# Kernel tuning notes

Hardware: AMD Instinct MI355X
Metric: run time of the kernel (lower is better)

The kernel has to match this reference:

```python
import jax, jax.numpy as jnp
import numpy as np

NUM_TOKENS = 8192
MODEL_DIM = 4096
NUM_EXPERTS = 64
CAPACITY_FACTOR = 1.0


def setup_inputs() -> dict:
    key = jax.random.key(0)
    k1, k2 = jax.random.split(key)
    inp = jax.random.normal(k1, (NUM_TOKENS, MODEL_DIM), dtype=jnp.float32)
    wg = jax.random.normal(k2, (NUM_EXPERTS, MODEL_DIM), dtype=jnp.float32) * (1.0 / np.sqrt(MODEL_DIM))
    return {"input": inp, "wg_weight": wg}


def reference(input, wg_weight):
    # logits = input @ wg.T  -> [T, E]
    logits = jnp.einsum('td,ed->te', input, wg_weight)
    num_tokens, num_experts = logits.shape
    capacity = int(CAPACITY_FACTOR * ((num_tokens + num_experts - 1) // num_experts))

    indices1_s = jnp.argmax(logits, axis=1)                      # [T]
    mask1 = jax.nn.one_hot(indices1_s, num_experts, dtype=logits.dtype)  # [T, E]
    gates = jax.nn.softmax(logits, axis=1)                       # [T, E]
    gates1_s = jnp.sum(gates * mask1, axis=1)                    # [T]

    # locations: position of each token within its chosen expert's queue
    # (exclusive cumsum over the one-hot mask, gathered at the chosen expert)
    locations1 = jnp.cumsum(mask1, axis=0) - 1.0                 # [T, E]
    locations1_s = jnp.sum(locations1 * mask1, axis=1).astype(jnp.int32)  # [T]

    # load-balancing aux loss (float32 branch of the original)
    me = jnp.sum(gates, axis=0)                                  # [E]
    ce = jnp.sum(mask1, axis=0)                                  # [E]
    l_aux = jnp.sum(me * ce) * (num_experts / (num_tokens * num_tokens))

    return (l_aux, indices1_s.astype(jnp.int32), locations1_s, gates1_s)
```

## Files before the change

kernel.cpp:

```cpp
#include <hip/hip_runtime.h>

namespace {
constexpr int TOK = 8192;
constexpr int DIM = 4096;
constexpr int NE  = 64;
constexpr int TB  = 128;
constexpr int KS  = 8;
constexpr int KR  = DIM / KS;
constexpr int NKS = KR / 32;
constexpr int TOTKS = DIM / 32;
constexpr int NT  = TOK / TB;
constexpr int GB  = 64;
constexpr int NCH = TOK / GB;
}

typedef _Float16 f16x8 __attribute__((ext_vector_type(8)));
typedef float    f32x4 __attribute__((ext_vector_type(4)));

__global__ __launch_bounds__(256) void prepack_w(
    const float* __restrict__ W, f16x8* __restrict__ whi,
    f16x8* __restrict__ wlo) {
  const int gid = blockIdx.x * 256 + threadIdx.x;
  const int lane = gid & 63;
  const int gk   = (gid >> 6) & (TOTKS - 1);
  const int et   = gid >> 13;
  const int e = et * 16 + (lane & 15);
  const int k = gk * 32 + (lane >> 4) * 8;
  const float4 r0 = *(const float4*)(W + (size_t)e * DIM + k);
  const float4 r1 = *(const float4*)(W + (size_t)e * DIM + k + 4);
  f16x8 hi, lo;
  const float rv[8] = {r0.x, r0.y, r0.z, r0.w, r1.x, r1.y, r1.z, r1.w};
#pragma unroll
  for (int j = 0; j < 8; ++j) {
    const _Float16 h = (_Float16)rv[j];
    hi[j] = h;
    lo[j] = (_Float16)(rv[j] - (float)h);
  }
  whi[gid] = hi;
  wlo[gid] = lo;
}

__global__ __launch_bounds__(512, 4) void gemm_split(
    const float* __restrict__ A, const _Float16* __restrict__ whi,
    const _Float16* __restrict__ wlo, float* __restrict__ partial) {
  __shared__ _Float16 sB[8 * 8 * 64 * 8];

  const int bid  = blockIdx.x;
  const int tile = bid & (NT - 1);
  const int ks   = bid / NT;
  const int t0   = tile * TB;
  const int tid  = threadIdx.x;
  const int w    = tid >> 6;
  const int lane = tid & 63;
  const int col  = lane & 15;
  const int quad = lane >> 4;
  const int gk0  = ks * NKS;

  const float* Ap = A + (size_t)(t0 + w * 16 + col) * DIM + ks * KR + quad * 8;

  f32x4 acc[4];
#pragma unroll
  for (int et = 0; et < 4; ++et) acc[et] = (f32x4)0.0f;

  float4 a0  = *(const float4*)(Ap);
  float4 a1  = *(const float4*)(Ap + 4);
  float4 a0n = *(const float4*)(Ap + 32);
  float4 a1n = *(const float4*)(Ap + 36);

  const _Float16* src_base =
      ((w < 4) ? whi : wlo) + ((size_t)((w & 3) * TOTKS + gk0) << 9);
  _Float16* dst_base = sB + ((size_t)w << 12);

  for (int half = 0; half < 2; ++half) {
    if (half) __syncthreads();
#pragma unroll
    for (int i = 0; i < 8; ++i) {
      const _Float16* src = src_base + (((size_t)(half * 8 + i)) << 9) + lane * 8;
      _Float16* dst = dst_base + ((size_t)i << 9) + lane * 8;
      __builtin_amdgcn_global_load_lds(
          (const __attribute__((address_space(1))) void*)src,
          (__attribute__((address_space(3))) void*)dst, 16, 0, 0);
    }
    __syncthreads();

    for (int s = 0; s < 8; ++s) {
      const int it = half * 8 + s;
      float4 a0nn, a1nn;
      if (it + 2 < NKS) {
        a0nn = *(const float4*)(Ap + (it + 2) * 32);
        a1nn = *(const float4*)(Ap + (it + 2) * 32 + 4);
      }
      const float av[8] = {a0.x, a0.y, a0.z, a0.w, a1.x, a1.y, a1.z, a1.w};
      f16x8 ah, al;
#pragma unroll
      for (int j = 0; j < 8; ++j) {
        const _Float16 h = (_Float16)av[j];
        ah[j] = h;
        al[j] = (_Float16)(av[j] - (float)h);
      }
#pragma unroll
      for (int et = 0; et < 4; ++et) {
        const f16x8 bh = *(const f16x8*)(sB + ((et * 8 + s) << 9) + lane * 8);
        const f16x8 bl =
            *(const f16x8*)(sB + (((4 + et) * 8 + s) << 9) + lane * 8);
        acc[et] = __builtin_amdgcn_mfma_f32_16x16x32_f16(ah, bh, acc[et], 0, 0, 0);
        acc[et] = __builtin_amdgcn_mfma_f32_16x16x32_f16(ah, bl, acc[et], 0, 0, 0);
        acc[et] = __builtin_amdgcn_mfma_f32_16x16x32_f16(al, bh, acc[et], 0, 0, 0);
      }
      a0 = a0n; a1 = a1n; a0n = a0nn; a1n = a1nn;
    }
  }

  float* P = partial + (size_t)ks * TOK * NE;
  const int tb = t0 + w * 16 + quad * 4;
#pragma unroll
  for (int et = 0; et < 4; ++et) {
    const int e = et * 16 + col;
#pragma unroll
    for (int r = 0; r < 4; ++r)
      P[(size_t)(tb + r) * NE + e] = acc[et][r];
  }
}

__global__ __launch_bounds__(256) void gating(
    const float* __restrict__ partial, float* __restrict__ out,
    int* __restrict__ idx_int, int* __restrict__ rankp,
    int* __restrict__ hist, float* __restrict__ me_part) {
  __shared__ float L[GB * 65];
  __shared__ float mx[GB];
  __shared__ float dninv[GB];
  __shared__ int   eid[GB];
  const int b = blockIdx.x, tid = threadIdx.x;
  const size_t base = (size_t)b * GB * NE;

#pragma unroll
  for (int j = 0; j < (GB * NE) / 256; ++j) {
    const int idx = tid + 256 * j;
    float s = 0.0f;
#pragma unroll
    for (int k = 0; k < KS; ++k)
      s += partial[(size_t)k * TOK * NE + base + idx];
    L[(idx >> 6) * 65 + (idx & 63)] = s;
  }
  __syncthreads();

  if (tid < GB) {
    const int t = tid;
    float m = -3.0e38f; int bi = 0;
    for (int e = 0; e < NE; ++e) {
      const float v = L[t * 65 + e];
      if (v > m) { m = v; bi = e; }
    }
    float s = 0.0f;
    for (int e = 0; e < NE; ++e) s += __expf(L[t * 65 + e] - m);
    const float inv = 1.0f / s;
    mx[t] = m; dninv[t] = inv; eid[t] = bi;
    const int gt = b * GB + t;
    out[1 + gt]           = (float)bi;
    out[1 + 2 * TOK + gt] = inv;
    idx_int[gt] = bi;
  }
  __syncthreads();

  if (tid < GB) {
    const int t = tid, e = eid[t];
    int r = 0;
    for (int j = 0; j < t; ++j) r += (eid[j] == e) ? 1 : 0;
    rankp[b * GB + t] = r;
    int c = 0;
    for (int t2 = 0; t2 < GB; ++t2) c += (eid[t2] == tid) ? 1 : 0;
    hist[b * NE + tid] = c;
  } else if (tid < 2 * GB) {
    const int e = tid - GB;
    float s = 0.0f;
    for (int t2 = 0; t2 < GB; ++t2)
      s += __expf(L[t2 * 65 + e] - mx[t2]) * dninv[t2];
    me_part[b * NE + e] = s;
  }
}

__global__ __launch_bounds__(256) void finalize(
    const int* __restrict__ idx_int, const int* __restrict__ rankp,
    const int* __restrict__ hist, const float* __restrict__ me_part,
    float* __restrict__ out) {
  __shared__ int   H[NCH * NE];
  __shared__ int   SEG[4 * NE];
  __shared__ float MEp[4 * NE];
  __shared__ float CE[NE];
  const int tid = threadIdx.x;
  const int e = tid & 63, seg = tid >> 6;

  for (int j = tid; j < NCH * NE; j += 256) H[j] = hist[j];
  {
    float s = 0.0f;
    for (int c = seg * 32; c < seg * 32 + 32; ++c) s += me_part[c * NE + e];
    MEp[seg * NE + e] = s;
  }
  __syncthreads();
  {
    int hs = 0;
    for (int c = seg * 32; c < seg * 32 + 32; ++c) hs += H[c * NE + e];
    SEG[seg * NE + e] = hs;
  }
  __syncthreads();
  if (tid < NE) {
    int run = 0;
    for (int s2 = 0; s2 < 4; ++s2) {
      const int v = SEG[s2 * NE + tid];
      SEG[s2 * NE + tid] = run;
      run += v;
    }
    CE[tid] = (float)run;
  }
  __syncthreads();
  {
    int run = SEG[seg * NE + e];
    for (int c = seg * 32; c < seg * 32 + 32; ++c) {
      const int v = H[c * NE + e];
      H[c * NE + e] = run;
      run += v;
    }
  }
  if (tid < 64) {
    float p = (MEp[tid] + MEp[NE + tid] + MEp[2 * NE + tid] + MEp[3 * NE + tid])
              * CE[tid];
#pragma unroll
    for (int off = 32; off > 0; off >>= 1) p += __shfl_down(p, off);
    if (tid == 0) out[0] = p * ((float)NE / ((float)TOK * (float)TOK));
  }
  __syncthreads();
#pragma unroll 4
  for (int i = tid; i < TOK; i += 256) {
    const int ex = idx_int[i];
    out[1 + TOK + i] = (float)(H[(i >> 6) * NE + ex] + rankp[i]);
  }
}

extern "C" void kernel_launch(void* const* d_in, const int* in_sizes, int n_in,
                              void* d_out, int out_size, void* d_ws, size_t ws_size,
                              hipStream_t stream) {
  const float* A = (const float*)d_in[0];
  const float* W = (const float*)d_in[1];
  float* out = (float*)d_out;
  char* ws = (char*)d_ws;

  float* partial = (float*)ws;
  size_t off = (size_t)KS * TOK * NE * sizeof(float);
  _Float16* whi = (_Float16*)(ws + off);  off += (size_t)4 * TOTKS * 64 * 16;
  _Float16* wlo = (_Float16*)(ws + off);  off += (size_t)4 * TOTKS * 64 * 16;
  float* me_part = (float*)(ws + off);  off += (size_t)NCH * NE * sizeof(float);
  int* idx_int = (int*)(ws + off);      off += (size_t)TOK * sizeof(int);
  int* rankp   = (int*)(ws + off);      off += (size_t)TOK * sizeof(int);
  int* hist    = (int*)(ws + off);

  hipLaunchKernelGGL(prepack_w, dim3(128), dim3(256), 0, stream, W,
                     (f16x8*)whi, (f16x8*)wlo);
  hipLaunchKernelGGL(gemm_split, dim3(NT * KS), dim3(512), 0, stream,
                     A, whi, wlo, partial);
  hipLaunchKernelGGL(gating, dim3(NCH), dim3(256), 0, stream, partial, out,
                     idx_int, rankp, hist, me_part);
  hipLaunchKernelGGL(finalize, dim3(1), dim3(256), 0, stream, idx_int, rankp,
                     hist, me_part, out);
}
```

Baseline: 214.3 us.

## Fuse weight split into GEMM, halve K-split, parallelize gating and finalize

Removes the separate prepack kernel: each GEMM block now loads fp32 W directly, splits it into fp16 hi/lo and writes it to LDS itself. The K-split factor drops from 8 to 4, which halves the partial-sum traffic but leaves fewer blocks (256) for the GEMM grid. The gating kernel spreads argmax, softmax-denominator and expert-sum work across all 256 threads using vectorized partial reads. The finalize kernel moves to 1024 threads. In exchange, every GEMM block redoes the W conversion, and W is read without the async LDS load path.

After: 218.8 us. 1.02x slower.

```diff
diff --git a/kernel.cpp b/kernel.cpp
--- a/kernel.cpp
+++ b/kernel.cpp
@@ -5,10 +5,10 @@
 constexpr int DIM = 4096;
 constexpr int NE  = 64;
 constexpr int TB  = 128;
-constexpr int KS  = 8;
+constexpr int KS  = 4;
 constexpr int KR  = DIM / KS;
 constexpr int NKS = KR / 32;
-constexpr int TOTKS = DIM / 32;
+constexpr int NRND = NKS / 8;
 constexpr int NT  = TOK / TB;
 constexpr int GB  = 64;
 constexpr int NCH = TOK / GB;
@@ -17,32 +17,9 @@
 typedef _Float16 f16x8 __attribute__((ext_vector_type(8)));
 typedef float    f32x4 __attribute__((ext_vector_type(4)));
 
-__global__ __launch_bounds__(256) void prepack_w(
-    const float* __restrict__ W, f16x8* __restrict__ whi,
-    f16x8* __restrict__ wlo) {
-  const int gid = blockIdx.x * 256 + threadIdx.x;
-  const int lane = gid & 63;
-  const int gk   = (gid >> 6) & (TOTKS - 1);
-  const int et   = gid >> 13;
-  const int e = et * 16 + (lane & 15);
-  const int k = gk * 32 + (lane >> 4) * 8;
-  const float4 r0 = *(const float4*)(W + (size_t)e * DIM + k);
-  const float4 r1 = *(const float4*)(W + (size_t)e * DIM + k + 4);
-  f16x8 hi, lo;
-  const float rv[8] = {r0.x, r0.y, r0.z, r0.w, r1.x, r1.y, r1.z, r1.w};
-#pragma unroll
-  for (int j = 0; j < 8; ++j) {
-    const _Float16 h = (_Float16)rv[j];
-    hi[j] = h;
-    lo[j] = (_Float16)(rv[j] - (float)h);
-  }
-  whi[gid] = hi;
-  wlo[gid] = lo;
-}
-
 __global__ __launch_bounds__(512, 4) void gemm_split(
-    const float* __restrict__ A, const _Float16* __restrict__ whi,
-    const _Float16* __restrict__ wlo, float* __restrict__ partial) {
+    const float* __restrict__ A, const float* __restrict__ W,
+    float* __restrict__ partial) {
   __shared__ _Float16 sB[8 * 8 * 64 * 8];
 
   const int bid  = blockIdx.x;
@@ -54,7 +31,10 @@
   const int lane = tid & 63;
   const int col  = lane & 15;
   const int quad = lane >> 4;
-  const int gk0  = ks * NKS;
+
+  const int etw = w & 3;
+  const int s0  = (w >> 2) * 4;
+  const float* Wp = W + (size_t)(etw * 16 + col) * DIM + ks * KR + quad * 8;
 
   const float* Ap = A + (size_t)(t0 + w * 16 + col) * DIM + ks * KR + quad * 8;
 
@@ -67,24 +47,27 @@
   float4 a0n = *(const float4*)(Ap + 32);
   float4 a1n = *(const float4*)(Ap + 36);
 
-  const _Float16* src_base =
-      ((w < 4) ? whi : wlo) + ((size_t)((w & 3) * TOTKS + gk0) << 9);
-  _Float16* dst_base = sB + ((size_t)w << 12);
-
-  for (int half = 0; half < 2; ++half) {
-    if (half) __syncthreads();
-#pragma unroll
-    for (int i = 0; i < 8; ++i) {
-      const _Float16* src = src_base + (((size_t)(half * 8 + i)) << 9) + lane * 8;
-      _Float16* dst = dst_base + ((size_t)i << 9) + lane * 8;
-      __builtin_amdgcn_global_load_lds(
-          (const __attribute__((address_space(1))) void*)src,
-          (__attribute__((address_space(3))) void*)dst, 16, 0, 0);
+  for (int rnd = 0; rnd < NRND; ++rnd) {
+    if (rnd) __syncthreads();
+#pragma unroll
+    for (int s = s0; s < s0 + 4; ++s) {
+      const float4 w0 = *(const float4*)(Wp + (rnd * 8 + s) * 32);
+      const float4 w1 = *(const float4*)(Wp + (rnd * 8 + s) * 32 + 4);
+      const float wv[8] = {w0.x, w0.y, w0.z, w0.w, w1.x, w1.y, w1.z, w1.w};
+      f16x8 hi, lo;
+#pragma unroll
+      for (int j = 0; j < 8; ++j) {
+        const _Float16 h = (_Float16)wv[j];
+        hi[j] = h;
+        lo[j] = (_Float16)(wv[j] - (float)h);
+      }
+      *(f16x8*)(sB + ((etw * 8 + s) << 9) + lane * 8) = hi;
+      *(f16x8*)(sB + (((4 + etw) * 8 + s) << 9) + lane * 8) = lo;
     }
     __syncthreads();
 
     for (int s = 0; s < 8; ++s) {
-      const int it = half * 8 + s;
+      const int it = rnd * 8 + s;
       float4 a0nn, a1nn;
       if (it + 2 < NKS) {
         a0nn = *(const float4*)(Ap + (it + 2) * 32);
@@ -127,85 +110,118 @@
     int* __restrict__ idx_int, int* __restrict__ rankp,
     int* __restrict__ hist, float* __restrict__ me_part) {
   __shared__ float L[GB * 65];
+  __shared__ float pm[4][GB];
+  __shared__ int   pi[4][GB];
+  __shared__ float ps[4][GB];
+  __shared__ float mep[4][NE];
   __shared__ float mx[GB];
   __shared__ float dninv[GB];
   __shared__ int   eid[GB];
   const int b = blockIdx.x, tid = threadIdx.x;
+  const int t = tid & 63, q = tid >> 6;
   const size_t base = (size_t)b * GB * NE;
 
 #pragma unroll
-  for (int j = 0; j < (GB * NE) / 256; ++j) {
-    const int idx = tid + 256 * j;
-    float s = 0.0f;
-#pragma unroll
-    for (int k = 0; k < KS; ++k)
-      s += partial[(size_t)k * TOK * NE + base + idx];
-    L[(idx >> 6) * 65 + (idx & 63)] = s;
-  }
-  __syncthreads();
-
-  if (tid < GB) {
-    const int t = tid;
-    float m = -3.0e38f; int bi = 0;
-    for (int e = 0; e < NE; ++e) {
+  for (int j = 0; j < 4; ++j) {
+    const int i4 = tid + 256 * j;
+    const int tt = i4 >> 4, e4 = (i4 & 15) * 4;
+    f32x4 s = (f32x4)0.0f;
+#pragma unroll
+    for (int k = 0; k < KS; ++k) {
+      const f32x4 v = *(const f32x4*)(partial + (size_t)k * TOK * NE + base +
+                                      (size_t)tt * NE + e4);
+      s += v;
+    }
+    *(f32x4*)(L + tt * 65 + e4) = s;
+  }
+  __syncthreads();
+
+  {
+    float m = -3.0e38f; int bi = q * 16;
+#pragma unroll
+    for (int e = q * 16; e < q * 16 + 16; ++e) {
       const float v = L[t * 65 + e];
       if (v > m) { m = v; bi = e; }
     }
+    pm[q][t] = m; pi[q][t] = bi;
+  }
+  __syncthreads();
+  if (tid < GB) {
+    float m = -3.0e38f; int bi = 0;
+#pragma unroll
+    for (int qq = 0; qq < 4; ++qq) {
+      if (pm[qq][tid] > m) { m = pm[qq][tid]; bi = pi[qq][tid]; }
+    }
+    mx[tid] = m; eid[tid] = bi;
+    const int gt = b * GB + tid;
+    out[1 + gt] = (float)bi;
+    idx_int[gt] = bi;
+  }
+  __syncthreads();
+  {
+    const float m = mx[t];
     float s = 0.0f;
-    for (int e = 0; e < NE; ++e) s += __expf(L[t * 65 + e] - m);
-    const float inv = 1.0f / s;
-    mx[t] = m; dninv[t] = inv; eid[t] = bi;
-    const int gt = b * GB + t;
-    out[1 + gt]           = (float)bi;
-    out[1 + 2 * TOK + gt] = inv;
-    idx_int[gt] = bi;
-  }
-  __syncthreads();
-
+#pragma unroll
+    for (int e = q * 16; e < q * 16 + 16; ++e) s += __expf(L[t * 65 + e] - m);
+    ps[q][t] = s;
+  }
+  __syncthreads();
   if (tid < GB) {
-    const int t = tid, e = eid[t];
+    const float inv = 1.0f / (ps[0][tid] + ps[1][tid] + ps[2][tid] + ps[3][tid]);
+    dninv[tid] = inv;
+    out[1 + 2 * TOK + b * GB + tid] = inv;
+  }
+  __syncthreads();
+  {
+    const int e = t;
+    float s = 0.0f;
+#pragma unroll
+    for (int tt = q * 16; tt < q * 16 + 16; ++tt)
+      s += __expf(L[tt * 65 + e] - mx[tt]) * dninv[tt];
+    mep[q][e] = s;
+  }
+  __syncthreads();
+  if (tid < GB) {
+    const int e = eid[tid];
     int r = 0;
-    for (int j = 0; j < t; ++j) r += (eid[j] == e) ? 1 : 0;
-    rankp[b * GB + t] = r;
+    for (int j = 0; j < tid; ++j) r += (eid[j] == e) ? 1 : 0;
+    rankp[b * GB + tid] = r;
     int c = 0;
     for (int t2 = 0; t2 < GB; ++t2) c += (eid[t2] == tid) ? 1 : 0;
     hist[b * NE + tid] = c;
   } else if (tid < 2 * GB) {
     const int e = tid - GB;
-    float s = 0.0f;
-    for (int t2 = 0; t2 < GB; ++t2)
-      s += __expf(L[t2 * 65 + e] - mx[t2]) * dninv[t2];
-    me_part[b * NE + e] = s;
-  }
-}
-
-__global__ __launch_bounds__(256) void finalize(
+    me_part[b * NE + e] = mep[0][e] + mep[1][e] + mep[2][e] + mep[3][e];
+  }
+}
+
+__global__ __launch_bounds__(1024) void finalize(
     const int* __restrict__ idx_int, const int* __restrict__ rankp,
     const int* __restrict__ hist, const float* __restrict__ me_part,
     float* __restrict__ out) {
   __shared__ int   H[NCH * NE];
-  __shared__ int   SEG[4 * NE];
-  __shared__ float MEp[4 * NE];
+  __shared__ int   SEG[16 * NE];
+  __shared__ float MEp[16 * NE];
   __shared__ float CE[NE];
   const int tid = threadIdx.x;
   const int e = tid & 63, seg = tid >> 6;
 
-  for (int j = tid; j < NCH * NE; j += 256) H[j] = hist[j];
+  for (int j = tid; j < NCH * NE; j += 1024) H[j] = hist[j];
   {
     float s = 0.0f;
-    for (int c = seg * 32; c < seg * 32 + 32; ++c) s += me_part[c * NE + e];
+    for (int c = seg * 8; c < seg * 8 + 8; ++c) s += me_part[c * NE + e];
     MEp[seg * NE + e] = s;
   }
   __syncthreads();
   {
     int hs = 0;
-    for (int c = seg * 32; c < seg * 32 + 32; ++c) hs += H[c * NE + e];
+    for (int c = seg * 8; c < seg * 8 + 8; ++c) hs += H[c * NE + e];
     SEG[seg * NE + e] = hs;
   }
   __syncthreads();
   if (tid < NE) {
     int run = 0;
-    for (int s2 = 0; s2 < 4; ++s2) {
+    for (int s2 = 0; s2 < 16; ++s2) {
       const int v = SEG[s2 * NE + tid];
       SEG[s2 * NE + tid] = run;
       run += v;
@@ -215,22 +231,24 @@
   __syncthreads();
   {
     int run = SEG[seg * NE + e];
-    for (int c = seg * 32; c < seg * 32 + 32; ++c) {
+    for (int c = seg * 8; c < seg * 8 + 8; ++c) {
       const int v = H[c * NE + e];
       H[c * NE + e] = run;
       run += v;
     }
   }
   if (tid < 64) {
-    float p = (MEp[tid] + MEp[NE + tid] + MEp[2 * NE + tid] + MEp[3 * NE + tid])
-              * CE[tid];
+    float me = 0.0f;
+#pragma unroll
+    for (int s2 = 0; s2 < 16; ++s2) me += MEp[s2 * NE + tid];
+    float p = me * CE[tid];
 #pragma unroll
     for (int off = 32; off > 0; off >>= 1) p += __shfl_down(p, off);
     if (tid == 0) out[0] = p * ((float)NE / ((float)TOK * (float)TOK));
   }
   __syncthreads();
-#pragma unroll 4
-  for (int i = tid; i < TOK; i += 256) {
+#pragma unroll
+  for (int i = tid; i < TOK; i += 1024) {
     const int ex = idx_int[i];
     out[1 + TOK + i] = (float)(H[(i >> 6) * NE + ex] + rankp[i]);
   }
@@ -246,19 +264,15 @@
 
   float* partial = (float*)ws;
   size_t off = (size_t)KS * TOK * NE * sizeof(float);
-  _Float16* whi = (_Float16*)(ws + off);  off += (size_t)4 * TOTKS * 64 * 16;
-  _Float16* wlo = (_Float16*)(ws + off);  off += (size_t)4 * TOTKS * 64 * 16;
   float* me_part = (float*)(ws + off);  off += (size_t)NCH * NE * sizeof(float);
   int* idx_int = (int*)(ws + off);      off += (size_t)TOK * sizeof(int);
   int* rankp   = (int*)(ws + off);      off += (size_t)TOK * sizeof(int);
   int* hist    = (int*)(ws + off);
 
-  hipLaunchKernelGGL(prepack_w, dim3(128), dim3(256), 0, stream, W,
-                     (f16x8*)whi, (f16x8*)wlo);
   hipLaunchKernelGGL(gemm_split, dim3(NT * KS), dim3(512), 0, stream,
-                     A, whi, wlo, partial);
+                     A, W, partial);
   hipLaunchKernelGGL(gating, dim3(NCH), dim3(256), 0, stream, partial, out,
                      idx_int, rankp, hist, me_part);
-  hipLaunchKernelGGL(finalize, dim3(1), dim3(256), 0, stream, idx_int, rankp,
+  hipLaunchKernelGGL(finalize, dim3(1), dim3(1024), 0, stream, idx_int, rankp,
                      hist, me_part, out);
 }
```
